# Performance work log

Measured on AMD Instinct MI355X. Metric: run time of the kernel, lower is better.

The kernel has to match this reference:

```python
import math
import jax, jax.numpy as jnp
import numpy as np

B, T, D, H = 4, 1024, 1024, 8
HD = D // H  # head_dim = 128

def _trigram_dirs():
    # 8 trigrams = all sign combinations in {−1,+1}^3, L2-normalized (p=2, dim=1)
    t = np.array([[(i >> b & 1) * 2 - 1 for b in (2, 1, 0)] for i in range(8)], dtype=np.float32)
    return jnp.asarray(t / np.linalg.norm(t, axis=1, keepdims=True))

def setup_inputs() -> dict:
    key = jax.random.key(0)
    k1, k2, k3, k4 = jax.random.split(key, 4)
    x = jax.random.normal(k1, (B, T, D), dtype=jnp.float32)
    Wqkv = jax.random.normal(k2, (D, 3 * D), dtype=jnp.float32) * 0.02
    Wout = jax.random.normal(k3, (D, D), dtype=jnp.float32) * 0.02
    # head_scales init to 0 in the module; use nonzero values so the geo-bias path is exercised
    head_scales = jax.random.normal(k4, (H,), dtype=jnp.float32) * 0.1
    head_dirs = _trigram_dirs()  # [H, 3] buffer
    return {"x": x, "Wqkv": Wqkv, "Wout": Wout, "head_scales": head_scales, "head_dirs": head_dirs}

def reference(x, Wqkv, Wout, head_scales, head_dirs):
    b, t, d = x.shape
    scale = 1.0 / math.sqrt(HD)
    qkv = (x @ Wqkv).reshape(b, t, 3, H, HD)
    qkv = jnp.transpose(qkv, (2, 0, 3, 1, 4))  # [3, B, H, T, HD]
    q, k, v = qkv[0], qkv[1], qkv[2]
    # scores: [B, H, T, T]
    scores = jnp.einsum('bhqd,bhkd->bhqk', q, k) * scale
    # rank-1 trigram geometric bias from first 3 dims of q/k
    q_proj = jnp.einsum('bhtd,hd->bht', q[..., :3], head_dirs)
    k_proj = jnp.einsum('bhtd,hd->bht', k[..., :3], head_dirs)
    geo_bias = q_proj[..., :, None] * k_proj[..., None, :]  # [B, H, T, T]
    scores = scores + head_scales[None, :, None, None] * geo_bias
    causal = jnp.tril(jnp.ones((t, t), dtype=bool))
    scores = jnp.where(causal, scores, -jnp.inf)
    attn = jax.nn.softmax(scores, axis=-1)
    out = jnp.einsum('bhqk,bhkd->bhqd', attn, v)  # [B, H, T, HD]
    out = jnp.transpose(out, (0, 2, 1, 3)).reshape(b, t, d)
    return out @ Wout
```

## Files before the change

### kernel.cpp

```cpp
#include <hip/hip_runtime.h>
#include <stdint.h>

typedef __attribute__((ext_vector_type(8))) short short8;
typedef __attribute__((ext_vector_type(4))) short short4v;
typedef __attribute__((ext_vector_type(4))) float f32x4;

__device__ __forceinline__ short f2bf(float x) {
  union { float f; uint32_t u; } c; c.f = x;
  uint32_t r = (c.u + 0x7FFFu + ((c.u >> 16) & 1u)) >> 16;
  return (short)r;
}
__device__ __forceinline__ float b2f(short s) {
  union { uint32_t u; float f; } c; c.u = ((uint32_t)(uint16_t)s) << 16;
  return c.f;
}
__device__ __forceinline__ uint32_t pack2bf(float lo, float hi) {
  return ((uint32_t)(uint16_t)f2bf(hi) << 16) | (uint32_t)(uint16_t)f2bf(lo);
}

__global__ __launch_bounds__(256) void cvt_kernel(const float* __restrict__ in,
                                                  short* __restrict__ out, int n4) {
  int i = blockIdx.x * 256 + threadIdx.x;
  const int stride = gridDim.x * 256;
  for (; i < n4; i += stride) {
    float4 v = reinterpret_cast<const float4*>(in)[i];
    short4v o;
    o.x = f2bf(v.x); o.y = f2bf(v.y); o.z = f2bf(v.z); o.w = f2bf(v.w);
    reinterpret_cast<short4v*>(out)[i] = o;
  }
}

__global__ __launch_bounds__(256) void tcvt_kernel(const float* __restrict__ in,
                                                   short* __restrict__ out, int K, int N) {
  __shared__ __align__(16) short tile[32][33];
  const int nb = blockIdx.x * 32, kb = blockIdx.y * 32;
  const int tx = threadIdx.x & 31, ty = threadIdx.x >> 5;
#pragma unroll
  for (int i = 0; i < 32; i += 8)
    tile[ty + i][tx] = f2bf(in[(size_t)(kb + ty + i) * N + nb + tx]);
  __syncthreads();
#pragma unroll
  for (int i = 0; i < 32; i += 8)
    out[(size_t)(nb + ty + i) * K + kb + tx] = tile[tx][ty + i];
}

__global__ __launch_bounds__(256) void vtrans_kernel(const short* __restrict__ qkvb,
                                                     short* __restrict__ vT) {
  __shared__ __align__(16) short tile[64][65];
  const int b = blockIdx.z;
  const int kv0 = blockIdx.x * 64, c0 = blockIdx.y * 64;
  const int tx = threadIdx.x & 15, ty = threadIdx.x >> 4;
  const short* src = qkvb + (size_t)(b * 1024) * 3072 + 2048;
#pragma unroll
  for (int i = 0; i < 64; i += 16) {
    int r = ty + i;
#pragma unroll
    for (int j = 0; j < 4; ++j)
      tile[r][tx * 4 + j] = src[(size_t)(kv0 + r) * 3072 + c0 + tx * 4 + j];
  }
  __syncthreads();
  short* dst = vT + (size_t)b * 1024 * 1024;
#pragma unroll
  for (int i = 0; i < 64; i += 16) {
    int cc = ty + i;
#pragma unroll
    for (int j = 0; j < 4; ++j)
      dst[(size_t)(c0 + cc) * 1024 + kv0 + tx * 4 + j] = tile[tx * 4 + j][cc];
  }
}

__global__ __launch_bounds__(256) void kproj_kernel(const short* __restrict__ qkvb,
                                                    const float* __restrict__ hdirs,
                                                    float* __restrict__ kproj) {
  const int i = blockIdx.x * 256 + threadIdx.x;
  const int bh = i >> 10, tt = i & 1023;
  const int b = bh >> 3, h = bh & 7;
  const float d0 = hdirs[h * 3], d1 = hdirs[h * 3 + 1], d2 = hdirs[h * 3 + 2];
  const short* kr = qkvb + (size_t)(b * 1024 + tt) * 3072 + 1024 + h * 128;
  kproj[i] = b2f(kr[0]) * d0 + b2f(kr[1]) * d1 + b2f(kr[2]) * d2;
}

template <int OUT_BF16>
__global__ __launch_bounds__(256) void gemm_kernel(const short* __restrict__ A,
                                                   const short* __restrict__ Bt,
                                                   void* __restrict__ Cout,
                                                   int K, int ldc) {
  __shared__ __align__(16) short Al[2][128 * 32];
  __shared__ __align__(16) short Bl[2][128 * 32];
  const int t = threadIdx.x;
  const int lane = t & 63, w = t >> 6;
  const int wr = w >> 1, wc = w & 1;
  const int g = lane >> 4, c16 = lane & 15;
  const int row0 = blockIdx.y * 128, col0 = blockIdx.x * 128;

  f32x4 acc[4][4];
#pragma unroll
  for (int m = 0; m < 4; ++m)
#pragma unroll
    for (int n = 0; n < 4; ++n) {
      f32x4 z = {0.0f, 0.0f, 0.0f, 0.0f};
      acc[m][n] = z;
    }

  auto stage = [&](int buf, int kt) {
    const int k0 = kt * 32;
#pragma unroll
    for (int i = 0; i < 2; ++i) {
      const int qb = i * 256 + (t & 192);
      const int q = qb + lane;
      const int r = q >> 2;
      const int c = (q & 3) ^ ((r >> 1) & 3);
      const short* ga = A + (size_t)(row0 + r) * K + k0 + c * 8;
      const short* gb = Bt + (size_t)(col0 + r) * K + k0 + c * 8;
      __builtin_amdgcn_global_load_lds((const __attribute__((address_space(1))) void*)ga,
                                       (__attribute__((address_space(3))) void*)&Al[buf][qb * 8],
                                       16, 0, 0);
      __builtin_amdgcn_global_load_lds((const __attribute__((address_space(1))) void*)gb,
                                       (__attribute__((address_space(3))) void*)&Bl[buf][qb * 8],
                                       16, 0, 0);
    }
  };

  stage(0, 0);
  __syncthreads();
  const int NK = K >> 5;
  int cur = 0;
  const int rA0 = wr * 64 + c16;
  const int rB0 = wc * 64 + c16;
  for (int kt = 0; kt < NK; ++kt) {
    if (kt + 1 < NK) stage(cur ^ 1, kt + 1);
    short8 aF[4], bF[4];
#pragma unroll
    for (int m = 0; m < 4; ++m) {
      const int r = rA0 + m * 16;
      const int c = g ^ ((r >> 1) & 3);
      aF[m] = *reinterpret_cast<const short8*>(&Al[cur][r * 32 + c * 8]);
    }
#pragma unroll
    for (int n = 0; n < 4; ++n) {
      const int r = rB0 + n * 16;
      const int c = g ^ ((r >> 1) & 3);
      bF[n] = *reinterpret_cast<const short8*>(&Bl[cur][r * 32 + c * 8]);
    }
#pragma unroll
    for (int m = 0; m < 4; ++m)
#pragma unroll
      for (int n = 0; n < 4; ++n)
        acc[m][n] = __builtin_amdgcn_mfma_f32_16x16x32_bf16(aF[m], bF[n], acc[m][n], 0, 0, 0);
    __syncthreads();
    cur ^= 1;
  }

  const int er = row0 + wr * 64 + g * 4;
  const int ec = col0 + wc * 64 + c16;
#pragma unroll
  for (int m = 0; m < 4; ++m)
#pragma unroll
    for (int n = 0; n < 4; ++n)
#pragma unroll
      for (int j = 0; j < 4; ++j) {
        const size_t off = (size_t)(er + m * 16 + j) * ldc + ec + n * 16;
        if (OUT_BF16)
          ((short*)Cout)[off] = f2bf(acc[m][n][j]);
        else
          ((float*)Cout)[off] = acc[m][n][j];
      }
}

template <int OUT_BF16>
__global__ __launch_bounds__(256) void gemm64_kernel(const short* __restrict__ A,
                                                     const short* __restrict__ Bt,
                                                     void* __restrict__ Cout,
                                                     int K, int ldc) {
  __shared__ __align__(16) short Al[2][128 * 32];
  __shared__ __align__(16) short Bl[2][64 * 32];
  const int t = threadIdx.x;
  const int lane = t & 63, w = t >> 6;
  const int wr = w >> 1, wc = w & 1;
  const int g = lane >> 4, c16 = lane & 15;
  const int row0 = blockIdx.y * 128, col0 = blockIdx.x * 64;

  f32x4 acc[4][2];
#pragma unroll
  for (int m = 0; m < 4; ++m)
#pragma unroll
    for (int n = 0; n < 2; ++n) {
      f32x4 z = {0.0f, 0.0f, 0.0f, 0.0f};
      acc[m][n] = z;
    }

  auto stage = [&](int buf, int kt) {
    const int k0 = kt * 32;
#pragma unroll
    for (int i = 0; i < 2; ++i) {
      const int qb = i * 256 + (t & 192);
      const int q = qb + lane;
      const int r = q >> 2;
      const int c = (q & 3) ^ ((r >> 1) & 3);
      const short* ga = A + (size_t)(row0 + r) * K + k0 + c * 8;
      __builtin_amdgcn_global_load_lds((const __attribute__((address_space(1))) void*)ga,
                                       (__attribute__((address_space(3))) void*)&Al[buf][qb * 8],
                                       16, 0, 0);
    }
    {
      const int qb = (t & 192);
      const int q = qb + lane;
      const int r = q >> 2;
      const int c = (q & 3) ^ ((r >> 1) & 3);
      const short* gb = Bt + (size_t)(col0 + r) * K + k0 + c * 8;
      __builtin_amdgcn_global_load_lds((const __attribute__((address_space(1))) void*)gb,
                                       (__attribute__((address_space(3))) void*)&Bl[buf][qb * 8],
                                       16, 0, 0);
    }
  };

  stage(0, 0);
  __syncthreads();
  const int NK = K >> 5;
  int cur = 0;
  const int rA0 = wr * 64 + c16;
  const int rB0 = wc * 32 + c16;
  for (int kt = 0; kt < NK; ++kt) {
    if (kt + 1 < NK) stage(cur ^ 1, kt + 1);
    short8 aF[4], bF[2];
#pragma unroll
    for (int m = 0; m < 4; ++m) {
      const int r = rA0 + m * 16;
      const int c = g ^ ((r >> 1) & 3);
      aF[m] = *reinterpret_cast<const short8*>(&Al[cur][r * 32 + c * 8]);
    }
#pragma unroll
    for (int n = 0; n < 2; ++n) {
      const int r = rB0 + n * 16;
      const int c = g ^ ((r >> 1) & 3);
      bF[n] = *reinterpret_cast<const short8*>(&Bl[cur][r * 32 + c * 8]);
    }
#pragma unroll
    for (int m = 0; m < 4; ++m)
#pragma unroll
      for (int n = 0; n < 2; ++n)
        acc[m][n] = __builtin_amdgcn_mfma_f32_16x16x32_bf16(aF[m], bF[n], acc[m][n], 0, 0, 0);
    __syncthreads();
    cur ^= 1;
  }

  const int er = row0 + wr * 64 + g * 4;
  const int ec = col0 + wc * 32 + c16;
#pragma unroll
  for (int m = 0; m < 4; ++m)
#pragma unroll
    for (int n = 0; n < 2; ++n)
#pragma unroll
      for (int j = 0; j < 4; ++j) {
        const size_t off = (size_t)(er + m * 16 + j) * ldc + ec + n * 16;
        if (OUT_BF16)
          ((short*)Cout)[off] = f2bf(acc[m][n][j]);
        else
          ((float*)Cout)[off] = acc[m][n][j];
      }
}

__global__ __launch_bounds__(256) void attn_kernel(const short* __restrict__ qkvb,
                                                   const short* __restrict__ vT,
                                                   const float* __restrict__ head_scales,
                                                   const float* __restrict__ hdirs,
                                                   const float* __restrict__ kproj,
                                                   short* __restrict__ attnb) {
  __shared__ __align__(16) short Kl[2][64 * 128];
  __shared__ __align__(16) short Vl[2][128 * 64];
  __shared__ float kp_lds[2][64];

  const int bid = blockIdx.x;
  const int bh = (bid & 7) * 4 + ((bid >> 3) & 3);
  const int r2 = bid >> 5;
  const int qt = (bid < 256) ? (15 - r2) : (r2 - 8);
  const int b = bh >> 3, h = bh & 7;
  const int t = threadIdx.x, lane = t & 63, w = t >> 6;
  const int g = lane >> 4, c16 = lane & 15;
  const int q0w = qt * 64 + w * 16;
  const int q_abs = q0w + c16;

  const short* qbase = qkvb + (size_t)(b * 1024) * 3072 + h * 128;
  const short* kbase = qbase + 1024;
  const short* vtb = vT + (size_t)bh * 128 * 1024;
  const float* kp = kproj + bh * 1024;

  const float LOG2E = 1.44269504088896f;
  const float scale2 = 0.08838834764831845f * 1.44269504088896f;

  short8 aQ[4];
  float hqp;
  {
    const short* qr = qbase + (size_t)(q0w + c16) * 3072;
#pragma unroll
    for (int kk = 0; kk < 4; ++kk)
      aQ[kk] = *reinterpret_cast<const short8*>(qr + kk * 32 + g * 8);
    const float hs = head_scales[h];
    hqp = hs * LOG2E *
          (b2f(qr[0]) * hdirs[h * 3] + b2f(qr[1]) * hdirs[h * 3 + 1] + b2f(qr[2]) * hdirs[h * 3 + 2]);
  }

  float m_s = -1e30f, l_s = 0.0f;
  f32x4 accO[8];
#pragma unroll
  for (int d = 0; d < 8; ++d) {
    f32x4 z = {0.0f, 0.0f, 0.0f, 0.0f};
    accO[d] = z;
  }

  auto stageKV = [&](int buf, int kvt) {
    const int kv0 = kvt * 64;
#pragma unroll
    for (int i = 0; i < 4; ++i) {
      const int s = w * 4 + i;
      {
        const int r = s * 4 + g;
        const int c = c16 ^ (r & 7);
        const short* ga = kbase + (size_t)(kv0 + r) * 3072 + c * 8;
        __builtin_amdgcn_global_load_lds((const __attribute__((address_space(1))) void*)ga,
                                         (__attribute__((address_space(3))) void*)&Kl[buf][s * 512],
                                         16, 0, 0);
      }
      {
        const int r = s * 8 + (lane >> 3);
        const int c = (lane & 7) ^ (r & 7);
        const short* ga = vtb + (size_t)r * 1024 + kv0 + c * 8;
        __builtin_amdgcn_global_load_lds((const __attribute__((address_space(1))) void*)ga,
                                         (__attribute__((address_space(3))) void*)&Vl[buf][s * 512],
                                         16, 0, 0);
      }
    }
    if (lane < 16) kp_lds[buf][w * 16 + lane] = kp[kv0 + w * 16 + lane];
  };

  const int nkv = qt + 1;
  stageKV(0, 0);
  __syncthreads();
  int cur = 0;
  for (int kvt = 0; kvt < nkv; ++kvt) {
    const int kv0 = kvt * 64;
    if (kvt + 1 < nkv) stageKV(cur ^ 1, kvt + 1);
    const short* Kc = Kl[cur];
    const short* Vc = Vl[cur];
    const float* kpc = kp_lds[cur];

    float p[4][4];
#pragma unroll
    for (int n = 0; n < 4; ++n) {
      f32x4 s4 = {0.0f, 0.0f, 0.0f, 0.0f};
      const int r = n * 16 + c16;
#pragma unroll
      for (int kk = 0; kk < 4; ++kk) {
        const int cch = (kk * 4 + g) ^ (r & 7);
        short8 bK = *reinterpret_cast<const short8*>(&Kc[r * 128 + cch * 8]);
        s4 = __builtin_amdgcn_mfma_f32_16x16x32_bf16(bK, aQ[kk], s4, 0, 0, 0);
      }
#pragma unroll
      for (int j = 0; j < 4; ++j) {
        const int kloc = n * 16 + g * 4 + j;
        const float v = s4[j] * scale2 + hqp * kpc[kloc];
        p[n][j] = (kv0 + kloc <= q_abs) ? v : -1e30f;
      }
    }

    float mx;
    {
      float a0 = fmaxf(fmaxf(p[0][0], p[0][1]), fmaxf(p[0][2], p[0][3]));
      float a1 = fmaxf(fmaxf(p[1][0], p[1][1]), fmaxf(p[1][2], p[1][3]));
      float a2 = fmaxf(fmaxf(p[2][0], p[2][1]), fmaxf(p[2][2], p[2][3]));
      float a3 = fmaxf(fmaxf(p[3][0], p[3][1]), fmaxf(p[3][2], p[3][3]));
      mx = fmaxf(fmaxf(a0, a1), fmaxf(a2, a3));
      mx = fmaxf(mx, __shfl_xor(mx, 16, 64));
      mx = fmaxf(mx, __shfl_xor(mx, 32, 64));
    }

    if (__any(mx - m_s > 11.54f)) {
      const float mn = fmaxf(m_s, mx);
      const float alpha = exp2f(m_s - mn);
      m_s = mn;
      l_s *= alpha;
      float aO[4];
#pragma unroll
      for (int j = 0; j < 4; ++j) aO[j] = __shfl(alpha, g * 4 + j, 64);
#pragma unroll
      for (int d = 0; d < 8; ++d)
#pragma unroll
        for (int j = 0; j < 4; ++j) accO[d][j] *= aO[j];
    }

    float s01 = 0.0f, s23 = 0.0f;
#pragma unroll
    for (int n = 0; n < 4; ++n) {
      float e0 = exp2f(p[n][0] - m_s), e1 = exp2f(p[n][1] - m_s);
      float e2 = exp2f(p[n][2] - m_s), e3 = exp2f(p[n][3] - m_s);
      p[n][0] = e0; p[n][1] = e1; p[n][2] = e2; p[n][3] = e3;
      if (n < 2) s01 += (e0 + e1) + (e2 + e3); else s23 += (e0 + e1) + (e2 + e3);
    }
    float sum = s01 + s23;
    sum += __shfl_xor(sum, 16, 64);
    sum += __shfl_xor(sum, 32, 64);
    l_s += sum;

    uint32_t pk[4][2];
#pragma unroll
    for (int n = 0; n < 4; ++n) {
      pk[n][0] = pack2bf(p[n][0], p[n][1]);
      pk[n][1] = pack2bf(p[n][2], p[n][3]);
    }

    union { uint32_t d[4]; short8 s; } aPu[2];
#pragma unroll
    for (int kk = 0; kk < 2; ++kk)
#pragma unroll
      for (int wd = 0; wd < 4; ++wd) {
        const int src = (2 * (g & 1) + (wd >> 1)) * 16 + c16;
        const uint32_t v0 = (uint32_t)__shfl((int)pk[kk * 2][wd & 1], src, 64);
        const uint32_t v1 = (uint32_t)__shfl((int)pk[kk * 2 + 1][wd & 1], src, 64);
        aPu[kk].d[wd] = (g >= 2) ? v1 : v0;
      }

#pragma unroll
    for (int dt = 0; dt < 8; ++dt) {
      const int r = dt * 16 + c16;
#pragma unroll
      for (int kk = 0; kk < 2; ++kk) {
        const int cch = (kk * 4 + g) ^ (r & 7);
        short8 bV = *reinterpret_cast<const short8*>(&Vc[r * 64 + cch * 8]);
        accO[dt] = __builtin_amdgcn_mfma_f32_16x16x32_bf16(aPu[kk].s, bV, accO[dt], 0, 0, 0);
      }
    }
    __syncthreads();
    cur ^= 1;
  }

  float linv[4];
#pragma unroll
  for (int j = 0; j < 4; ++j) linv[j] = 1.0f / __shfl(l_s, g * 4 + j, 64);
#pragma unroll
  for (int j = 0; j < 4; ++j) {
    const size_t rowoff = (size_t)(b * 1024 + q0w + g * 4 + j) * 1024 + h * 128;
#pragma unroll
    for (int dt = 0; dt < 8; ++dt)
      attnb[rowoff + dt * 16 + c16] = f2bf(accO[dt][j] * linv[j]);
  }
}

extern "C" void kernel_launch(void* const* d_in, const int* in_sizes, int n_in,
                              void* d_out, int out_size, void* d_ws, size_t ws_size,
                              hipStream_t stream) {
  const float* x = (const float*)d_in[0];
  const float* Wqkv = (const float*)d_in[1];
  const float* Wout = (const float*)d_in[2];
  const float* hscale = (const float*)d_in[3];
  const float* hdirs = (const float*)d_in[4];
  float* out = (float*)d_out;

  char* ws = (char*)d_ws;
  short* xb = (short*)(ws);
  short* wqkvT = (short*)(ws + (size_t)8 * 1024 * 1024);
  short* woutT = (short*)(ws + (size_t)14 * 1024 * 1024);
  short* qkvb = (short*)(ws + (size_t)16 * 1024 * 1024);
  short* vT = (short*)(ws + (size_t)40 * 1024 * 1024);
  short* attnb = (short*)(ws + (size_t)48 * 1024 * 1024);
  float* kproj = (float*)(ws);

  cvt_kernel<<<2048, 256, 0, stream>>>(x, xb, (4 * 1024 * 1024) / 4);
  tcvt_kernel<<<dim3(96, 32), 256, 0, stream>>>(Wqkv, wqkvT, 1024, 3072);
  tcvt_kernel<<<dim3(32, 32), 256, 0, stream>>>(Wout, woutT, 1024, 1024);
  gemm_kernel<1><<<dim3(24, 32), 256, 0, stream>>>(xb, wqkvT, (void*)qkvb, 1024, 3072);
  kproj_kernel<<<128, 256, 0, stream>>>(qkvb, hdirs, kproj);
  vtrans_kernel<<<dim3(16, 16, 4), 256, 0, stream>>>(qkvb, vT);
  attn_kernel<<<512, 256, 0, stream>>>(qkvb, vT, hscale, hdirs, kproj, attnb);
  gemm64_kernel<0><<<dim3(16, 32), 256, 0, stream>>>(attnb, woutT, out, 1024, 1024);
}
```

Baseline: 116.3 us.

## Split attention KV loop across two wave groups and fuse prep kernels

The attention kernel now runs 512 threads per block. Two groups of four waves each process alternating KV tiles for the same query rows, and their partial softmax states (max, sum, output) are merged through shared memory at the end. The old double-buffer prefetch is dropped in favour of each half staging its own tile. The three input-conversion kernels are fused into one launch, and V-transpose plus k-projection are fused into another, to cut launch overhead. The intent is to halve the serial KV loop length per block, at the cost of the merge step, losing the load/compute overlap, and higher register/LDS pressure per block.

```diff
diff --git a/kernel.cpp b/kernel.cpp
--- a/kernel.cpp
+++ b/kernel.cpp
@@ -18,66 +18,81 @@
   return ((uint32_t)(uint16_t)f2bf(hi) << 16) | (uint32_t)(uint16_t)f2bf(lo);
 }
 
-__global__ __launch_bounds__(256) void cvt_kernel(const float* __restrict__ in,
-                                                  short* __restrict__ out, int n4) {
-  int i = blockIdx.x * 256 + threadIdx.x;
-  const int stride = gridDim.x * 256;
-  for (; i < n4; i += stride) {
-    float4 v = reinterpret_cast<const float4*>(in)[i];
-    short4v o;
-    o.x = f2bf(v.x); o.y = f2bf(v.y); o.z = f2bf(v.z); o.w = f2bf(v.w);
-    reinterpret_cast<short4v*>(out)[i] = o;
-  }
-}
-
-__global__ __launch_bounds__(256) void tcvt_kernel(const float* __restrict__ in,
-                                                   short* __restrict__ out, int K, int N) {
+__global__ __launch_bounds__(256) void prep_kernel(const float* __restrict__ x,
+                                                   const float* __restrict__ Wqkv,
+                                                   const float* __restrict__ Wout,
+                                                   short* __restrict__ xb,
+                                                   short* __restrict__ wqkvT,
+                                                   short* __restrict__ woutT) {
   __shared__ __align__(16) short tile[32][33];
-  const int nb = blockIdx.x * 32, kb = blockIdx.y * 32;
-  const int tx = threadIdx.x & 31, ty = threadIdx.x >> 5;
-#pragma unroll
-  for (int i = 0; i < 32; i += 8)
-    tile[ty + i][tx] = f2bf(in[(size_t)(kb + ty + i) * N + nb + tx]);
-  __syncthreads();
-#pragma unroll
-  for (int i = 0; i < 32; i += 8)
-    out[(size_t)(nb + ty + i) * K + kb + tx] = tile[tx][ty + i];
-}
-
-__global__ __launch_bounds__(256) void vtrans_kernel(const short* __restrict__ qkvb,
-                                                     short* __restrict__ vT) {
+  const int bid = blockIdx.x;
+  if (bid < 2048) {
+    const int n4 = (4 * 1024 * 1024) / 4;
+    int i = bid * 256 + threadIdx.x;
+    for (; i < n4; i += 2048 * 256) {
+      float4 v = reinterpret_cast<const float4*>(x)[i];
+      short4v o;
+      o.x = f2bf(v.x); o.y = f2bf(v.y); o.z = f2bf(v.z); o.w = f2bf(v.w);
+      reinterpret_cast<short4v*>(xb)[i] = o;
+    }
+  } else {
+    const float* in;
+    short* out;
+    int K, N, bx, by;
+    if (bid < 2048 + 3072) {
+      const int idx = bid - 2048;
+      in = Wqkv; out = wqkvT; K = 1024; N = 3072; bx = idx % 96; by = idx / 96;
+    } else {
+      const int idx = bid - 5120;
+      in = Wout; out = woutT; K = 1024; N = 1024; bx = idx % 32; by = idx / 32;
+    }
+    const int nb = bx * 32, kb = by * 32;
+    const int tx = threadIdx.x & 31, ty = threadIdx.x >> 5;
+#pragma unroll
+    for (int i = 0; i < 32; i += 8)
+      tile[ty + i][tx] = f2bf(in[(size_t)(kb + ty + i) * N + nb + tx]);
+    __syncthreads();
+#pragma unroll
+    for (int i = 0; i < 32; i += 8)
+      out[(size_t)(nb + ty + i) * K + kb + tx] = tile[tx][ty + i];
+  }
+}
+
+__global__ __launch_bounds__(256) void kvprep_kernel(const short* __restrict__ qkvb,
+                                                     const float* __restrict__ hdirs,
+                                                     short* __restrict__ vT,
+                                                     float* __restrict__ kproj) {
   __shared__ __align__(16) short tile[64][65];
-  const int b = blockIdx.z;
-  const int kv0 = blockIdx.x * 64, c0 = blockIdx.y * 64;
-  const int tx = threadIdx.x & 15, ty = threadIdx.x >> 4;
-  const short* src = qkvb + (size_t)(b * 1024) * 3072 + 2048;
-#pragma unroll
-  for (int i = 0; i < 64; i += 16) {
-    int r = ty + i;
-#pragma unroll
-    for (int j = 0; j < 4; ++j)
-      tile[r][tx * 4 + j] = src[(size_t)(kv0 + r) * 3072 + c0 + tx * 4 + j];
-  }
-  __syncthreads();
-  short* dst = vT + (size_t)b * 1024 * 1024;
-#pragma unroll
-  for (int i = 0; i < 64; i += 16) {
-    int cc = ty + i;
-#pragma unroll
-    for (int j = 0; j < 4; ++j)
-      dst[(size_t)(c0 + cc) * 1024 + kv0 + tx * 4 + j] = tile[tx * 4 + j][cc];
-  }
-}
-
-__global__ __launch_bounds__(256) void kproj_kernel(const short* __restrict__ qkvb,
-                                                    const float* __restrict__ hdirs,
-                                                    float* __restrict__ kproj) {
-  const int i = blockIdx.x * 256 + threadIdx.x;
-  const int bh = i >> 10, tt = i & 1023;
-  const int b = bh >> 3, h = bh & 7;
-  const float d0 = hdirs[h * 3], d1 = hdirs[h * 3 + 1], d2 = hdirs[h * 3 + 2];
-  const short* kr = qkvb + (size_t)(b * 1024 + tt) * 3072 + 1024 + h * 128;
-  kproj[i] = b2f(kr[0]) * d0 + b2f(kr[1]) * d1 + b2f(kr[2]) * d2;
+  const int bid = blockIdx.x;
+  if (bid < 1024) {
+    const int b = bid / 256;
+    const int kv0 = (bid % 16) * 64, c0 = ((bid / 16) % 16) * 64;
+    const int tx = threadIdx.x & 15, ty = threadIdx.x >> 4;
+    const short* src = qkvb + (size_t)(b * 1024) * 3072 + 2048;
+#pragma unroll
+    for (int i = 0; i < 64; i += 16) {
+      int r = ty + i;
+#pragma unroll
+      for (int j = 0; j < 4; ++j)
+        tile[r][tx * 4 + j] = src[(size_t)(kv0 + r) * 3072 + c0 + tx * 4 + j];
+    }
+    __syncthreads();
+    short* dst = vT + (size_t)b * 1024 * 1024;
+#pragma unroll
+    for (int i = 0; i < 64; i += 16) {
+      int cc = ty + i;
+#pragma unroll
+      for (int j = 0; j < 4; ++j)
+        dst[(size_t)(c0 + cc) * 1024 + kv0 + tx * 4 + j] = tile[tx * 4 + j][cc];
+    }
+  } else {
+    const int i = (bid - 1024) * 256 + threadIdx.x;
+    const int bh = i >> 10, tt = i & 1023;
+    const int b = bh >> 3, h = bh & 7;
+    const float d0 = hdirs[h * 3], d1 = hdirs[h * 3 + 1], d2 = hdirs[h * 3 + 2];
+    const short* kr = qkvb + (size_t)(b * 1024 + tt) * 3072 + 1024 + h * 128;
+    kproj[i] = b2f(kr[0]) * d0 + b2f(kr[1]) * d1 + b2f(kr[2]) * d2;
+  }
 }
 
 template <int OUT_BF16>
@@ -260,15 +275,24 @@
       }
 }
 
-__global__ __launch_bounds__(256) void attn_kernel(const short* __restrict__ qkvb,
+struct AttnSmem {
+  union {
+    struct {
+      short Kl[2][64 * 128];
+      short Vl[2][128 * 64];
+      float kp[2][64];
+    } s;
+    float mg[4 * 64 * 34];
+  };
+};
+
+__global__ __launch_bounds__(512) void attn_kernel(const short* __restrict__ qkvb,
                                                    const short* __restrict__ vT,
                                                    const float* __restrict__ head_scales,
                                                    const float* __restrict__ hdirs,
                                                    const float* __restrict__ kproj,
                                                    short* __restrict__ attnb) {
-  __shared__ __align__(16) short Kl[2][64 * 128];
-  __shared__ __align__(16) short Vl[2][128 * 64];
-  __shared__ float kp_lds[2][64];
+  __shared__ __align__(16) AttnSmem sm;
 
   const int bid = blockIdx.x;
   const int bh = (bid & 7) * 4 + ((bid >> 3) & 3);
@@ -276,8 +300,9 @@
   const int qt = (bid < 256) ? (15 - r2) : (r2 - 8);
   const int b = bh >> 3, h = bh & 7;
   const int t = threadIdx.x, lane = t & 63, w = t >> 6;
+  const int half = w >> 2, wq = w & 3;
   const int g = lane >> 4, c16 = lane & 15;
-  const int q0w = qt * 64 + w * 16;
+  const int q0w = qt * 64 + wq * 16;
   const int q_abs = q0w + c16;
 
   const short* qbase = qkvb + (size_t)(b * 1024) * 3072 + h * 128;
@@ -308,17 +333,17 @@
     accO[d] = z;
   }
 
-  auto stageKV = [&](int buf, int kvt) {
+  auto stageKV = [&](int set, int kvt) {
     const int kv0 = kvt * 64;
 #pragma unroll
     for (int i = 0; i < 4; ++i) {
-      const int s = w * 4 + i;
+      const int s = wq * 4 + i;
       {
         const int r = s * 4 + g;
         const int c = c16 ^ (r & 7);
         const short* ga = kbase + (size_t)(kv0 + r) * 3072 + c * 8;
         __builtin_amdgcn_global_load_lds((const __attribute__((address_space(1))) void*)ga,
-                                         (__attribute__((address_space(3))) void*)&Kl[buf][s * 512],
+                                         (__attribute__((address_space(3))) void*)&sm.s.Kl[set][s * 512],
                                          16, 0, 0);
       }
       {
@@ -326,122 +351,152 @@
         const int c = (lane & 7) ^ (r & 7);
         const short* ga = vtb + (size_t)r * 1024 + kv0 + c * 8;
         __builtin_amdgcn_global_load_lds((const __attribute__((address_space(1))) void*)ga,
-                                         (__attribute__((address_space(3))) void*)&Vl[buf][s * 512],
+                                         (__attribute__((address_space(3))) void*)&sm.s.Vl[set][s * 512],
                                          16, 0, 0);
       }
     }
-    if (lane < 16) kp_lds[buf][w * 16 + lane] = kp[kv0 + w * 16 + lane];
+    if (lane < 16) sm.s.kp[set][wq * 16 + lane] = kp[kv0 + wq * 16 + lane];
   };
 
   const int nkv = qt + 1;
-  stageKV(0, 0);
+  const int nsteps = (nkv + 1) >> 1;
+  for (int st = 0; st < nsteps; ++st) {
+    const int tile = 2 * st + half;
+    const bool active = tile < nkv;
+    if (active) stageKV(half, tile);
+    __syncthreads();
+    if (active) {
+      const int kv0 = tile * 64;
+      const short* Kc = sm.s.Kl[half];
+      const short* Vc = sm.s.Vl[half];
+      const float* kpc = sm.s.kp[half];
+      const int nmax = (tile == qt) ? (wq + 1) : 4;
+
+      float p[4][4];
+#pragma unroll
+      for (int n = 0; n < 4; ++n) {
+        if (n < nmax) {
+          f32x4 s4 = {0.0f, 0.0f, 0.0f, 0.0f};
+          const int r = n * 16 + c16;
+#pragma unroll
+          for (int kk = 0; kk < 4; ++kk) {
+            const int cch = (kk * 4 + g) ^ (r & 7);
+            short8 bK = *reinterpret_cast<const short8*>(&Kc[r * 128 + cch * 8]);
+            s4 = __builtin_amdgcn_mfma_f32_16x16x32_bf16(bK, aQ[kk], s4, 0, 0, 0);
+          }
+#pragma unroll
+          for (int j = 0; j < 4; ++j) {
+            const int kloc = n * 16 + g * 4 + j;
+            const float v = s4[j] * scale2 + hqp * kpc[kloc];
+            p[n][j] = (kv0 + kloc <= q_abs) ? v : -1e30f;
+          }
+        } else {
+          p[n][0] = -1e30f; p[n][1] = -1e30f; p[n][2] = -1e30f; p[n][3] = -1e30f;
+        }
+      }
+
+      float mx;
+      {
+        float a0 = fmaxf(fmaxf(p[0][0], p[0][1]), fmaxf(p[0][2], p[0][3]));
+        float a1 = fmaxf(fmaxf(p[1][0], p[1][1]), fmaxf(p[1][2], p[1][3]));
+        float a2 = fmaxf(fmaxf(p[2][0], p[2][1]), fmaxf(p[2][2], p[2][3]));
+        float a3 = fmaxf(fmaxf(p[3][0], p[3][1]), fmaxf(p[3][2], p[3][3]));
+        mx = fmaxf(fmaxf(a0, a1), fmaxf(a2, a3));
+        mx = fmaxf(mx, __shfl_xor(mx, 16, 64));
+        mx = fmaxf(mx, __shfl_xor(mx, 32, 64));
+      }
+
+      if (__any(mx - m_s > 11.54f)) {
+        const float mn = fmaxf(m_s, mx);
+        const float alpha = exp2f(m_s - mn);
+        m_s = mn;
+        l_s *= alpha;
+        float aO[4];
+#pragma unroll
+        for (int j = 0; j < 4; ++j) aO[j] = __shfl(alpha, g * 4 + j, 64);
+#pragma unroll
+        for (int d = 0; d < 8; ++d)
+#pragma unroll
+          for (int j = 0; j < 4; ++j) accO[d][j] *= aO[j];
+      }
+
+      float s01 = 0.0f, s23 = 0.0f;
+#pragma unroll
+      for (int n = 0; n < 4; ++n) {
+        float e0 = exp2f(p[n][0] - m_s), e1 = exp2f(p[n][1] - m_s);
+        float e2 = exp2f(p[n][2] - m_s), e3 = exp2f(p[n][3] - m_s);
+        p[n][0] = e0; p[n][1] = e1; p[n][2] = e2; p[n][3] = e3;
+        if (n < 2) s01 += (e0 + e1) + (e2 + e3); else s23 += (e0 + e1) + (e2 + e3);
+      }
+      float sum = s01 + s23;
+      sum += __shfl_xor(sum, 16, 64);
+      sum += __shfl_xor(sum, 32, 64);
+      l_s += sum;
+
+      uint32_t pk[4][2];
+#pragma unroll
+      for (int n = 0; n < 4; ++n) {
+        pk[n][0] = pack2bf(p[n][0], p[n][1]);
+        pk[n][1] = pack2bf(p[n][2], p[n][3]);
+      }
+
+      union { uint32_t d[4]; short8 s; } aPu[2];
+#pragma unroll
+      for (int kk = 0; kk < 2; ++kk)
+#pragma unroll
+        for (int wd = 0; wd < 4; ++wd) {
+          const int src = (2 * (g & 1) + (wd >> 1)) * 16 + c16;
+          const uint32_t v0 = (uint32_t)__shfl((int)pk[kk * 2][wd & 1], src, 64);
+          const uint32_t v1 = (uint32_t)__shfl((int)pk[kk * 2 + 1][wd & 1], src, 64);
+          aPu[kk].d[wd] = (g >= 2) ? v1 : v0;
+        }
+
+#pragma unroll
+      for (int dt = 0; dt < 8; ++dt) {
+        const int r = dt * 16 + c16;
+#pragma unroll
+        for (int kk = 0; kk < 2; ++kk) {
+          const int cch = (kk * 4 + g) ^ (r & 7);
+          short8 bV = *reinterpret_cast<const short8*>(&Vc[r * 64 + cch * 8]);
+          accO[dt] = __builtin_amdgcn_mfma_f32_16x16x32_bf16(aPu[kk].s, bV, accO[dt], 0, 0, 0);
+        }
+      }
+    }
+    __syncthreads();
+  }
+
+  if (half == 1) {
+    float* pd = sm.mg + (size_t)(wq * 64 + lane) * 34;
+    pd[0] = m_s;
+    pd[1] = l_s;
+#pragma unroll
+    for (int d = 0; d < 8; ++d)
+#pragma unroll
+      for (int j = 0; j < 4; ++j) pd[2 + d * 4 + j] = accO[d][j];
+  }
   __syncthreads();
-  int cur = 0;
-  for (int kvt = 0; kvt < nkv; ++kvt) {
-    const int kv0 = kvt * 64;
-    if (kvt + 1 < nkv) stageKV(cur ^ 1, kvt + 1);
-    const short* Kc = Kl[cur];
-    const short* Vc = Vl[cur];
-    const float* kpc = kp_lds[cur];
-
-    float p[4][4];
-#pragma unroll
-    for (int n = 0; n < 4; ++n) {
-      f32x4 s4 = {0.0f, 0.0f, 0.0f, 0.0f};
-      const int r = n * 16 + c16;
-#pragma unroll
-      for (int kk = 0; kk < 4; ++kk) {
-        const int cch = (kk * 4 + g) ^ (r & 7);
-        short8 bK = *reinterpret_cast<const short8*>(&Kc[r * 128 + cch * 8]);
-        s4 = __builtin_amdgcn_mfma_f32_16x16x32_bf16(bK, aQ[kk], s4, 0, 0, 0);
-      }
-#pragma unroll
-      for (int j = 0; j < 4; ++j) {
-        const int kloc = n * 16 + g * 4 + j;
-        const float v = s4[j] * scale2 + hqp * kpc[kloc];
-        p[n][j] = (kv0 + kloc <= q_abs) ? v : -1e30f;
-      }
-    }
-
-    float mx;
-    {
-      float a0 = fmaxf(fmaxf(p[0][0], p[0][1]), fmaxf(p[0][2], p[0][3]));
-      float a1 = fmaxf(fmaxf(p[1][0], p[1][1]), fmaxf(p[1][2], p[1][3]));
-      float a2 = fmaxf(fmaxf(p[2][0], p[2][1]), fmaxf(p[2][2], p[2][3]));
-      float a3 = fmaxf(fmaxf(p[3][0], p[3][1]), fmaxf(p[3][2], p[3][3]));
-      mx = fmaxf(fmaxf(a0, a1), fmaxf(a2, a3));
-      mx = fmaxf(mx, __shfl_xor(mx, 16, 64));
-      mx = fmaxf(mx, __shfl_xor(mx, 32, 64));
-    }
-
-    if (__any(mx - m_s > 11.54f)) {
-      const float mn = fmaxf(m_s, mx);
-      const float alpha = exp2f(m_s - mn);
-      m_s = mn;
-      l_s *= alpha;
-      float aO[4];
-#pragma unroll
-      for (int j = 0; j < 4; ++j) aO[j] = __shfl(alpha, g * 4 + j, 64);
-#pragma unroll
-      for (int d = 0; d < 8; ++d)
-#pragma unroll
-        for (int j = 0; j < 4; ++j) accO[d][j] *= aO[j];
-    }
-
-    float s01 = 0.0f, s23 = 0.0f;
-#pragma unroll
-    for (int n = 0; n < 4; ++n) {
-      float e0 = exp2f(p[n][0] - m_s), e1 = exp2f(p[n][1] - m_s);
-      float e2 = exp2f(p[n][2] - m_s), e3 = exp2f(p[n][3] - m_s);
-      p[n][0] = e0; p[n][1] = e1; p[n][2] = e2; p[n][3] = e3;
-      if (n < 2) s01 += (e0 + e1) + (e2 + e3); else s23 += (e0 + e1) + (e2 + e3);
-    }
-    float sum = s01 + s23;
-    sum += __shfl_xor(sum, 16, 64);
-    sum += __shfl_xor(sum, 32, 64);
-    l_s += sum;
-
-    uint32_t pk[4][2];
-#pragma unroll
-    for (int n = 0; n < 4; ++n) {
-      pk[n][0] = pack2bf(p[n][0], p[n][1]);
-      pk[n][1] = pack2bf(p[n][2], p[n][3]);
-    }
-
-    union { uint32_t d[4]; short8 s; } aPu[2];
-#pragma unroll
-    for (int kk = 0; kk < 2; ++kk)
-#pragma unroll
-      for (int wd = 0; wd < 4; ++wd) {
-        const int src = (2 * (g & 1) + (wd >> 1)) * 16 + c16;
-        const uint32_t v0 = (uint32_t)__shfl((int)pk[kk * 2][wd & 1], src, 64);
-        const uint32_t v1 = (uint32_t)__shfl((int)pk[kk * 2 + 1][wd & 1], src, 64);
-        aPu[kk].d[wd] = (g >= 2) ? v1 : v0;
-      }
-
-#pragma unroll
-    for (int dt = 0; dt < 8; ++dt) {
-      const int r = dt * 16 + c16;
-#pragma unroll
-      for (int kk = 0; kk < 2; ++kk) {
-        const int cch = (kk * 4 + g) ^ (r & 7);
-        short8 bV = *reinterpret_cast<const short8*>(&Vc[r * 64 + cch * 8]);
-        accO[dt] = __builtin_amdgcn_mfma_f32_16x16x32_bf16(aPu[kk].s, bV, accO[dt], 0, 0, 0);
-      }
-    }
-    __syncthreads();
-    cur ^= 1;
-  }
-
-  float linv[4];
-#pragma unroll
-  for (int j = 0; j < 4; ++j) linv[j] = 1.0f / __shfl(l_s, g * 4 + j, 64);
-#pragma unroll
-  for (int j = 0; j < 4; ++j) {
-    const size_t rowoff = (size_t)(b * 1024 + q0w + g * 4 + j) * 1024 + h * 128;
-#pragma unroll
-    for (int dt = 0; dt < 8; ++dt)
-      attnb[rowoff + dt * 16 + c16] = f2bf(accO[dt][j] * linv[j]);
+  if (half == 0) {
+    const float* ps = sm.mg + (size_t)(wq * 64 + lane) * 34;
+    const float m1 = ps[0], l1 = ps[1];
+    const float mn = fmaxf(m_s, m1);
+    const float a0 = exp2f(m_s - mn), a1 = exp2f(m1 - mn);
+    const float lt = l_s * a0 + l1 * a1;
+    float sa0[4], sa1[4], linv[4];
+#pragma unroll
+    for (int j = 0; j < 4; ++j) {
+      sa0[j] = __shfl(a0, g * 4 + j, 64);
+      sa1[j] = __shfl(a1, g * 4 + j, 64);
+      linv[j] = 1.0f / __shfl(lt, g * 4 + j, 64);
+    }
+#pragma unroll
+    for (int j = 0; j < 4; ++j) {
+      const size_t rowoff = (size_t)(b * 1024 + q0w + g * 4 + j) * 1024 + h * 128;
+#pragma unroll
+      for (int dt = 0; dt < 8; ++dt) {
+        const float o1 = ps[2 + dt * 4 + j];
+        attnb[rowoff + dt * 16 + c16] = f2bf((accO[dt][j] * sa0[j] + o1 * sa1[j]) * linv[j]);
+      }
+    }
   }
 }
 
@@ -464,12 +519,9 @@
   short* attnb = (short*)(ws + (size_t)48 * 1024 * 1024);
   float* kproj = (float*)(ws);
 
-  cvt_kernel<<<2048, 256, 0, stream>>>(x, xb, (4 * 1024 * 1024) / 4);
-  tcvt_kernel<<<dim3(96, 32), 256, 0, stream>>>(Wqkv, wqkvT, 1024, 3072);
-  tcvt_kernel<<<dim3(32, 32), 256, 0, stream>>>(Wout, woutT, 1024, 1024);
+  prep_kernel<<<6144, 256, 0, stream>>>(x, Wqkv, Wout, xb, wqkvT, woutT);
   gemm_kernel<1><<<dim3(24, 32), 256, 0, stream>>>(xb, wqkvT, (void*)qkvb, 1024, 3072);
-  kproj_kernel<<<128, 256, 0, stream>>>(qkvb, hdirs, kproj);
-  vtrans_kernel<<<dim3(16, 16, 4), 256, 0, stream>>>(qkvb, vT);
-  attn_kernel<<<512, 256, 0, stream>>>(qkvb, vT, hscale, hdirs, kproj, attnb);
+  kvprep_kernel<<<1152, 256, 0, stream>>>(qkvb, hdirs, vT, kproj);
+  attn_kernel<<<512, 512, 0, stream>>>(qkvb, vT, hscale, hdirs, kproj, attnb);
   gemm64_kernel<0><<<dim3(16, 32), 256, 0, stream>>>(attnb, woutT, out, 1024, 1024);
 }
```

Result: faster. 111.6 us (-4.0%).
